# Optimization experiments

Measured on AMD Instinct MI355X. Metric: run time of the kernel, lower is better.

## Reference

```python
import jax, jax.numpy as jnp
from jax import lax
import numpy as np
import math

DIM = 192
D_INNER = DIM * 2            # 384
DT_RANK = math.ceil(DIM / 16)  # 12
D_STATE = 16
B, H, W = 4, 64, 64
KCONV = 4


def setup_inputs() -> dict:
    key = jax.random.key(0)
    ks = jax.random.split(key, 8)
    s = lambda k, shape, fan: jax.random.normal(k, shape, jnp.float32) / np.sqrt(fan).astype(np.float32)
    return {
        "x": jax.random.normal(ks[0], (B, DIM, H, W), jnp.float32),
        "W_in": s(ks[1], (2 * D_INNER, DIM), DIM),          # in_proj weight
        "conv_w": s(ks[2], (D_INNER, 1, KCONV), KCONV),     # depthwise conv weight
        "conv_b": jnp.zeros((D_INNER,), jnp.float32),
        "W_x": s(ks[3], (DT_RANK + 2 * D_STATE, D_INNER), D_INNER),  # x_proj weight
        "W_dt": s(ks[4], (D_INNER, DT_RANK), DT_RANK),      # dt_proj weight
        "b_dt": jax.random.uniform(ks[5], (D_INNER,), jnp.float32, -4.0, -2.0),  # dt_proj bias
        "A_log": jnp.tile(jnp.log(jnp.arange(1, D_STATE + 1, dtype=jnp.float32)), (D_INNER, 1)),
        "D": jnp.ones((D_INNER,), jnp.float32),
        "W_out": s(ks[6], (DIM, D_INNER), D_INNER),         # out_proj weight
    }


def _forward(x, W_in, conv_w, conv_b, W_x, W_dt, b_dt, A_log, D, W_out):
    Bb, C, Hh, Ww = x.shape
    L = Hh * Ww
    x_flat = x.reshape(Bb, C, L).transpose(0, 2, 1)        # (B, L, C)
    xz = x_flat @ W_in.T                                    # (B, L, 2*d_inner)
    x_in, z_gate = jnp.split(xz, 2, axis=-1)

    # depthwise causal conv1d: padding=3 on both sides in torch, then truncated
    # to first L outputs == left-pad-3 'VALID' conv with kernel 4.
    xt = x_in.transpose(0, 2, 1)                            # (B, d_inner, L)
    xt_pad = jnp.pad(xt, ((0, 0), (0, 0), (KCONV - 1, 0)))
    xc = lax.conv_general_dilated(
        xt_pad, conv_w, window_strides=(1,), padding="VALID",
        feature_group_count=D_INNER) + conv_b[None, :, None]
    x_conv = jax.nn.silu(xc)                                # (B, d_inner, L)

    x_dbl = jnp.einsum("bdl,kd->blk", x_conv, W_x)          # (B, L, dt_rank+32)
    dt, B_ssm, C_ssm = jnp.split(x_dbl, [DT_RANK, DT_RANK + D_STATE], axis=-1)

    # NOTE: dt_proj applies its bias AND delta_bias=dt_proj.bias is passed to the
    # scan, so the bias is added twice before softplus (faithful to source).
    dt_lin = dt @ W_dt.T + b_dt                             # (B, L, d_inner)
    delta = jax.nn.softplus(dt_lin + b_dt)

    A = -jnp.exp(A_log)                                     # (d_inner, d_state)

    # sequential selective scan over L
    def step(h, inp):
        u_t, d_t, B_t, C_t = inp                            # (B,d),(B,d),(B,n),(B,n)
        dA = jnp.exp(d_t[..., None] * A)                    # (B, d_inner, d_state)
        h = dA * h + (d_t * u_t)[..., None] * B_t[:, None, :]
        y_t = jnp.einsum("bdn,bn->bd", h, C_t)
        return h, y_t

    u_seq = x_conv.transpose(2, 0, 1)                       # (L, B, d_inner)
    d_seq = delta.transpose(1, 0, 2)                        # (L, B, d_inner)
    B_seq = B_ssm.transpose(1, 0, 2)                        # (L, B, d_state)
    C_seq = C_ssm.transpose(1, 0, 2)                        # (L, B, d_state)
    h0 = jnp.zeros((Bb, D_INNER, D_STATE), x.dtype)
    _, ys = lax.scan(step, h0, (u_seq, d_seq, B_seq, C_seq))  # (L, B, d_inner)

    y = ys.transpose(1, 2, 0) + D[None, :, None] * x_conv   # (B, d_inner, L)
    y = y * jax.nn.silu(z_gate.transpose(0, 2, 1))          # gate

    out = jnp.einsum("bdl,cd->bcl", y, W_out)               # out_proj
    return out.reshape(Bb, C, Hh, Ww)


def reference(x, W_in, conv_w, conv_b, W_x, W_dt, b_dt, A_log, D, W_out):
    return _forward(x, W_in, conv_w, conv_b, W_x, W_dt, b_dt, A_log, D, W_out)
```

## Files before the change

### kernel.cpp

```cpp
#include <hip/hip_runtime.h>
#include <hip/hip_bf16.h>
#include <math.h>

#define L_SEQ 4096
#define NB    4
#define DIMC  192
#define DIN   384
#define DIN2  768
#define DTRANK 12
#define DSTATE 16
#define NKX   44
#define G_CHUNKS 128
#define T_CHUNK  32
#define NCH  (NB*DIN*DSTATE)
#define NM   (NB*L_SEQ)
#define NBIG 448

typedef __attribute__((ext_vector_type(8))) short short8;
typedef __attribute__((ext_vector_type(4))) float floatx4;

__device__ __forceinline__ float silu_f(float v) {
    return v / (1.f + __expf(-v));
}
__device__ __forceinline__ float softplus_f(float v) {
    return fmaxf(v, 0.f) + __logf(1.f + __expf(-fabsf(v)));
}
__device__ __forceinline__ float bf2f(unsigned short u) {
    union { unsigned int i; float f; } c; c.i = ((unsigned int)u) << 16; return c.f;
}

__launch_bounds__(256)
__global__ void k_cvt_x(const float* __restrict__ x, __hip_bfloat16* __restrict__ xb) {
    __shared__ float s[32][33];
    const int b = blockIdx.z, c0 = blockIdx.y * 32, l0 = blockIdx.x * 32;
    const int tx = threadIdx.x, ty = threadIdx.y;
    const float* xp = x + ((size_t)b * DIMC + c0) * L_SEQ + l0;
#pragma unroll
    for (int r = 0; r < 4; ++r)
        s[ty + r*8][tx] = xp[(size_t)(ty + r*8) * L_SEQ + tx];
    __syncthreads();
    __hip_bfloat16* op = xb + ((size_t)b * L_SEQ + l0) * DIMC + c0;
#pragma unroll
    for (int r = 0; r < 4; ++r) {
        const int lr = ty + r*8;
        op[(size_t)lr * DIMC + tx] = __float2bfloat16(s[tx][lr]);
    }
}

#define NWI (DIN2*DIMC)
#define NWO (DIMC*DIN)
#define NWBIG (NBIG*DIN)
__launch_bounds__(256)
__global__ void k_cvt_w(const float* __restrict__ W_in, const float* __restrict__ W_out,
                        const float* __restrict__ W_x, const float* __restrict__ W_dt,
                        __hip_bfloat16* __restrict__ wbi, __hip_bfloat16* __restrict__ wbo,
                        __hip_bfloat16* __restrict__ wbig) {
    const int i = blockIdx.x * 256 + threadIdx.x;
    if (i < NWI) {
        wbi[i] = __float2bfloat16(W_in[i]);
    } else if (i < NWI + NWO) {
        const int j = i - NWI;
        wbo[j] = __float2bfloat16(W_out[j]);
    } else if (i < NWI + NWO + NWBIG) {
        const int j = i - NWI - NWO;
        const int r = j / DIN, c = j - r * DIN;
        float v;
        if (r < 32) {
            v = W_x[(size_t)(DTRANK + r) * DIN + c];
        } else if (r < 32 + DIN) {
            const int d = r - 32;
            v = 0.f;
#pragma unroll
            for (int q = 0; q < DTRANK; ++q)
                v += W_dt[d * DTRANK + q] * W_x[(size_t)q * DIN + c];
        } else {
            v = 0.f;
        }
        wbig[j] = __float2bfloat16(v);
    }
}

template<int BN, int OUTMODE>
__launch_bounds__(256)
__global__ void k_gemm(const __hip_bfloat16* __restrict__ A,
                       const __hip_bfloat16* __restrict__ B,
                       float* __restrict__ Cf, __hip_bfloat16* __restrict__ Cb,
                       float* __restrict__ Cf2, const float* __restrict__ bdt,
                       int K, int ldc) {
    constexpr int LDK = 200;
    constexpr int WN = BN / 2;
    constexpr int TN = WN / 16;
    constexpr int NCA = 6;
    constexpr int NCB = BN * 24 / 256;
    __shared__ __align__(16) __hip_bfloat16 sA[64 * LDK];
    __shared__ __align__(16) __hip_bfloat16 sB[BN * LDK];

    const int tid = threadIdx.x;
    const int lane = tid & 63;
    const int wave = tid >> 6;
    const int wm = wave >> 1, wn = wave & 1;
    const int m0 = blockIdx.x * 64;
    const int n0 = blockIdx.y * BN;
    const int mlan = lane & 15;
    const int kq8 = (lane >> 4) * 8;

    floatx4 acc[2][TN];
#pragma unroll
    for (int i = 0; i < 2; ++i)
#pragma unroll
        for (int j = 0; j < TN; ++j) acc[i][j] = (floatx4){0.f, 0.f, 0.f, 0.f};

    for (int kh = 0; kh < K; kh += 192) {
        if (kh) __syncthreads();
        uint4 va[NCA], vb[NCB];
#pragma unroll
        for (int r = 0; r < NCA; ++r) {
            const int c = r * 256 + tid, row = c / 24, cc = c - row * 24;
            va[r] = *(const uint4*)&A[(size_t)(m0 + row) * K + kh + cc * 8];
        }
#pragma unroll
        for (int r = 0; r < NCB; ++r) {
            const int c = r * 256 + tid, row = c / 24, cc = c - row * 24;
            vb[r] = *(const uint4*)&B[(size_t)(n0 + row) * K + kh + cc * 8];
        }
#pragma unroll
        for (int r = 0; r < NCA; ++r) {
            const int c = r * 256 + tid, row = c / 24, cc = c - row * 24;
            *(uint4*)&sA[row * LDK + cc * 8] = va[r];
        }
#pragma unroll
        for (int r = 0; r < NCB; ++r) {
            const int c = r * 256 + tid, row = c / 24, cc = c - row * 24;
            *(uint4*)&sB[row * LDK + cc * 8] = vb[r];
        }
        __syncthreads();
#pragma unroll
        for (int ks = 0; ks < 6; ++ks) {
            short8 af[2], bf[TN];
#pragma unroll
            for (int im = 0; im < 2; ++im)
                af[im] = *(const short8*)&sA[(wm*32 + im*16 + mlan) * LDK + ks*32 + kq8];
#pragma unroll
            for (int jn = 0; jn < TN; ++jn)
                bf[jn] = *(const short8*)&sB[(wn*WN + jn*16 + mlan) * LDK + ks*32 + kq8];
#pragma unroll
            for (int im = 0; im < 2; ++im)
#pragma unroll
                for (int jn = 0; jn < TN; ++jn)
                    acc[im][jn] = __builtin_amdgcn_mfma_f32_16x16x32_bf16(
                        af[im], bf[jn], acc[im][jn], 0, 0, 0);
        }
    }

    const int quad = lane >> 4;
#pragma unroll
    for (int im = 0; im < 2; ++im) {
#pragma unroll
        for (int jn = 0; jn < TN; ++jn) {
            const int n = n0 + wn*WN + jn*16 + mlan;
            const int mb = m0 + wm*32 + im*16 + quad*4;
#pragma unroll
            for (int r = 0; r < 4; ++r) {
                const int m = mb + r;
                const float v = acc[im][jn][r];
                if (OUTMODE == 0) {
                    Cb[(size_t)m * ldc + n] = __float2bfloat16(v);
                } else if (OUTMODE == 1) {
                    const int bb = m >> 12, ll = m & (L_SEQ - 1);
                    Cf[((size_t)bb * DIMC + n) * L_SEQ + ll] = v;
                } else {
                    if (n < 32) {
                        Cf[(size_t)m * 32 + n] = v;
                    } else if (n < 32 + DIN) {
                        Cf2[(size_t)m * DIN + (n - 32)] = softplus_f(v + 2.f * bdt[n - 32]);
                    }
                }
            }
        }
    }
}

__launch_bounds__(256)
__global__ void k_conv(const __hip_bfloat16* __restrict__ xz, const float* __restrict__ cw,
                       const float* __restrict__ cb, __hip_bfloat16* __restrict__ xcb) {
    const int idx = blockIdx.x * 256 + threadIdx.x;
    const int d = idx % DIN;
    const int m = idx / DIN;
    const int l = m & (L_SEQ - 1);
    const float4 w4 = *(const float4*)&cw[d * 4];
    float s = cb[d];
    const float w[4] = {w4.x, w4.y, w4.z, w4.w};
#pragma unroll
    for (int k = 0; k < 4; ++k) {
        const int ll = l - 3 + k;
        if (ll >= 0) s += __bfloat162float(xz[(size_t)(m - 3 + k) * DIN2 + d]) * w[k];
    }
    xcb[idx] = __float2bfloat16(silu_f(s));
}

__launch_bounds__(128)
__global__ void k_scan_a(const float* __restrict__ dlt, const __hip_bfloat16* __restrict__ xcb,
                         const float* __restrict__ xbc, const float* __restrict__ A_log,
                         float* __restrict__ S, float* __restrict__ P) {
    __shared__ float sBC[T_CHUNK * 32];
    const int tid = threadIdx.x;
    const int g = blockIdx.x, b = blockIdx.z;
    const int l0 = g * T_CHUNK;
    const size_t row0 = (size_t)b * L_SEQ + l0;
    for (int i = tid; i < T_CHUNK * 8; i += 128)
        *(float4*)&sBC[i * 4] = *(const float4*)&xbc[row0 * 32 + i * 4];
    const int d = blockIdx.y * 128 + tid;
    float dv_a[T_CHUNK];
    unsigned short uv_a[T_CHUNK];
#pragma unroll
    for (int t = 0; t < T_CHUNK; ++t)
        dv_a[t] = dlt[(row0 + t) * DIN + d];
#pragma unroll
    for (int t = 0; t < T_CHUNK; ++t)
        uv_a[t] = *(const unsigned short*)&xcb[(row0 + t) * DIN + d];
    float A[DSTATE];
#pragma unroll
    for (int n = 0; n < DSTATE; n += 4) {
        const float4 a4 = *(const float4*)&A_log[d * DSTATE + n];
        A[n] = -__expf(a4.x); A[n+1] = -__expf(a4.y);
        A[n+2] = -__expf(a4.z); A[n+3] = -__expf(a4.w);
    }
    __syncthreads();
    float h[DSTATE] = {};
    float dsum = 0.f;
#pragma unroll
    for (int t = 0; t < T_CHUNK; ++t) {
        const float dv = dv_a[t];
        const float uv = bf2f(uv_a[t]);
        const float dub = dv * uv;
        dsum += dv;
#pragma unroll
        for (int n = 0; n < DSTATE; ++n) {
            const float e = __expf(dv * A[n]);
            h[n] = e * h[n] + dub * sBC[t*32 + n];
        }
    }
    float* Sp = S + (size_t)g * NCH + (size_t)(b * DIN + d) * DSTATE;
    float* Pp = P + (size_t)g * NCH + (size_t)(b * DIN + d) * DSTATE;
#pragma unroll
    for (int n = 0; n < DSTATE; n += 4) {
        *(float4*)&Sp[n] = make_float4(h[n], h[n+1], h[n+2], h[n+3]);
        *(float4*)&Pp[n] = make_float4(__expf(A[n]*dsum), __expf(A[n+1]*dsum),
                                       __expf(A[n+2]*dsum), __expf(A[n+3]*dsum));
    }
}

__launch_bounds__(256)
__global__ void k_scan_b(float* __restrict__ Sh, const float* __restrict__ P) {
    const int ch = blockIdx.x * 256 + threadIdx.x;
    float h = 0.f;
    for (int g = 0; g < G_CHUNKS; ++g) {
        const size_t i = (size_t)g * NCH + ch;
        const float s = Sh[i];
        const float p = P[i];
        Sh[i] = h;
        h = p * h + s;
    }
}

__launch_bounds__(128)
__global__ void k_scan_c(const float* __restrict__ dlt, const __hip_bfloat16* __restrict__ xcb,
                         const float* __restrict__ xbc, const float* __restrict__ A_log,
                         const float* __restrict__ Hst, const __hip_bfloat16* __restrict__ xzb,
                         const float* __restrict__ Dv, __hip_bfloat16* __restrict__ yb) {
    __shared__ float sBC[T_CHUNK * 32];
    const int tid = threadIdx.x;
    const int g = blockIdx.x, b = blockIdx.z;
    const int l0 = g * T_CHUNK;
    const size_t row0 = (size_t)b * L_SEQ + l0;
    for (int i = tid; i < T_CHUNK * 8; i += 128)
        *(float4*)&sBC[i * 4] = *(const float4*)&xbc[row0 * 32 + i * 4];
    const int d = blockIdx.y * 128 + tid;
    float dv_a[T_CHUNK];
    unsigned short uv_a[T_CHUNK];
    unsigned short zz_a[T_CHUNK];
#pragma unroll
    for (int t = 0; t < T_CHUNK; ++t)
        dv_a[t] = dlt[(row0 + t) * DIN + d];
#pragma unroll
    for (int t = 0; t < T_CHUNK; ++t)
        uv_a[t] = *(const unsigned short*)&xcb[(row0 + t) * DIN + d];
#pragma unroll
    for (int t = 0; t < T_CHUNK; ++t)
        zz_a[t] = *(const unsigned short*)&xzb[(row0 + t) * DIN2 + DIN + d];
    float A[DSTATE];
#pragma unroll
    for (int n = 0; n < DSTATE; n += 4) {
        const float4 a4 = *(const float4*)&A_log[d * DSTATE + n];
        A[n] = -__expf(a4.x); A[n+1] = -__expf(a4.y);
        A[n+2] = -__expf(a4.z); A[n+3] = -__expf(a4.w);
    }
    float h[DSTATE];
    const float* Hp = Hst + (size_t)g * NCH + (size_t)(b * DIN + d) * DSTATE;
#pragma unroll
    for (int n = 0; n < DSTATE; n += 4) {
        const float4 h4 = *(const float4*)&Hp[n];
        h[n] = h4.x; h[n+1] = h4.y; h[n+2] = h4.z; h[n+3] = h4.w;
    }
    const float Dd = Dv[d];
    __hip_bfloat16* yl = yb + row0 * DIN + d;
    __syncthreads();
#pragma unroll
    for (int t = 0; t < T_CHUNK; ++t) {
        const float dv = dv_a[t];
        const float uv = bf2f(uv_a[t]);
        const float dub = dv * uv;
        float y0 = 0.f, y1 = 0.f, y2 = 0.f, y3 = 0.f;
#pragma unroll
        for (int n = 0; n < DSTATE; n += 4) {
            float e;
            e = __expf(dv * A[n  ]); h[n  ] = e * h[n  ] + dub * sBC[t*32 + n  ]; y0 += h[n  ] * sBC[t*32 + 16 + n  ];
            e = __expf(dv * A[n+1]); h[n+1] = e * h[n+1] + dub * sBC[t*32 + n+1]; y1 += h[n+1] * sBC[t*32 + 16 + n+1];
            e = __expf(dv * A[n+2]); h[n+2] = e * h[n+2] + dub * sBC[t*32 + n+2]; y2 += h[n+2] * sBC[t*32 + 16 + n+2];
            e = __expf(dv * A[n+3]); h[n+3] = e * h[n+3] + dub * sBC[t*32 + n+3]; y3 += h[n+3] * sBC[t*32 + 16 + n+3];
        }
        const float y = (y0 + y1) + (y2 + y3);
        yl[(size_t)t * DIN] = __float2bfloat16((y + Dd * uv) * silu_f(bf2f(zz_a[t])));
    }
}

extern "C" void kernel_launch(void* const* d_in, const int* in_sizes, int n_in,
                              void* d_out, int out_size, void* d_ws, size_t ws_size,
                              hipStream_t stream) {
    const float* x      = (const float*)d_in[0];
    const float* W_in   = (const float*)d_in[1];
    const float* conv_w = (const float*)d_in[2];
    const float* conv_b = (const float*)d_in[3];
    const float* W_x    = (const float*)d_in[4];
    const float* W_dt   = (const float*)d_in[5];
    const float* b_dt   = (const float*)d_in[6];
    const float* A_log  = (const float*)d_in[7];
    const float* Dvec   = (const float*)d_in[8];
    const float* W_out  = (const float*)d_in[9];
    float* out = (float*)d_out;

    char* p = (char*)d_ws;
    __hip_bfloat16* xb    = (__hip_bfloat16*)p; p += (size_t)NM * DIMC * 2;
    __hip_bfloat16* wbi   = (__hip_bfloat16*)p; p += (size_t)NWI * 2;
    __hip_bfloat16* wbo   = (__hip_bfloat16*)p; p += (size_t)NWO * 2;
    __hip_bfloat16* wbig  = (__hip_bfloat16*)p; p += (size_t)NWBIG * 2;
    __hip_bfloat16* xzb   = (__hip_bfloat16*)p; p += (size_t)NM * DIN2 * 2;
    __hip_bfloat16* xcb   = (__hip_bfloat16*)p; p += (size_t)NM * DIN * 2;
    float*          xbc   = (float*)p;          p += (size_t)NM * 32 * 4;
    float*          dlt   = (float*)p;          p += (size_t)NM * DIN * 4;
    __hip_bfloat16* yb    = (__hip_bfloat16*)p; p += (size_t)NM * DIN * 2;
    float*          S     = (float*)p;          p += (size_t)G_CHUNKS * NCH * 4;
    float*          P     = (float*)p;          p += (size_t)G_CHUNKS * NCH * 4;

    k_cvt_w<<<dim3((NWI + NWO + NWBIG + 255) / 256), 256, 0, stream>>>(
        W_in, W_out, W_x, W_dt, wbi, wbo, wbig);
    k_cvt_x<<<dim3(L_SEQ/32, DIMC/32, NB), dim3(32, 8), 0, stream>>>(x, xb);
    k_gemm<128, 0><<<dim3(NM/64, DIN2/128), 256, 0, stream>>>(
        xb, wbi, nullptr, xzb, nullptr, nullptr, DIMC, DIN2);
    k_conv<<<dim3((NM*(size_t)DIN)/256), 256, 0, stream>>>(xzb, conv_w, conv_b, xcb);
    k_gemm<64, 3><<<dim3(NM/64, NBIG/64), 256, 0, stream>>>(
        xcb, wbig, xbc, nullptr, dlt, b_dt, DIN, 0);
    k_scan_a<<<dim3(G_CHUNKS, 3, NB), 128, 0, stream>>>(dlt, xcb, xbc, A_log, S, P);
    k_scan_b<<<dim3(NCH/256), 256, 0, stream>>>(S, P);
    k_scan_c<<<dim3(G_CHUNKS, 3, NB), 128, 0, stream>>>(dlt, xcb, xbc, A_log,
                                                        S, xzb, Dvec, yb);
    k_gemm<96, 1><<<dim3(NM/64, DIMC/96), 256, 0, stream>>>(
        yb, wbo, out, nullptr, nullptr, nullptr, DIN, 0);
}
```

Measured before the change: 217.1 us.

## Fuse dt projection into scan kernels and fold x transpose into input GEMM

Removes the precomputed W_dt·W_x fused weight and the large fp32 delta buffer. The x_proj GEMM now writes only the 48-wide x_dbl, and both scan kernels compute delta in registers from the 12 dt-rank values with softplus. The separate x transpose/convert kernel is folded into the input GEMM, which loads fp32 x and transposes it into shared memory. This cuts a lot of global memory traffic, at the cost of recomputing the dt projection in both scan passes and doing strided scalar shared-memory stores in the input GEMM.

```diff
diff --git a/kernel.cpp b/kernel.cpp
--- a/kernel.cpp
+++ b/kernel.cpp
@@ -14,7 +14,7 @@
 #define T_CHUNK  32
 #define NCH  (NB*DIN*DSTATE)
 #define NM   (NB*L_SEQ)
-#define NBIG 448
+#define LDK  200
 
 typedef __attribute__((ext_vector_type(8))) short short8;
 typedef __attribute__((ext_vector_type(4))) float floatx4;
@@ -29,155 +29,94 @@
     union { unsigned int i; float f; } c; c.i = ((unsigned int)u) << 16; return c.f;
 }
 
-__launch_bounds__(256)
-__global__ void k_cvt_x(const float* __restrict__ x, __hip_bfloat16* __restrict__ xb) {
-    __shared__ float s[32][33];
-    const int b = blockIdx.z, c0 = blockIdx.y * 32, l0 = blockIdx.x * 32;
-    const int tx = threadIdx.x, ty = threadIdx.y;
-    const float* xp = x + ((size_t)b * DIMC + c0) * L_SEQ + l0;
-#pragma unroll
-    for (int r = 0; r < 4; ++r)
-        s[ty + r*8][tx] = xp[(size_t)(ty + r*8) * L_SEQ + tx];
-    __syncthreads();
-    __hip_bfloat16* op = xb + ((size_t)b * L_SEQ + l0) * DIMC + c0;
-#pragma unroll
-    for (int r = 0; r < 4; ++r) {
-        const int lr = ty + r*8;
-        op[(size_t)lr * DIMC + tx] = __float2bfloat16(s[tx][lr]);
-    }
-}
-
 #define NWI (DIN2*DIMC)
 #define NWO (DIMC*DIN)
-#define NWBIG (NBIG*DIN)
+#define NWX (64*DIN)
 __launch_bounds__(256)
 __global__ void k_cvt_w(const float* __restrict__ W_in, const float* __restrict__ W_out,
-                        const float* __restrict__ W_x, const float* __restrict__ W_dt,
+                        const float* __restrict__ W_x,
                         __hip_bfloat16* __restrict__ wbi, __hip_bfloat16* __restrict__ wbo,
-                        __hip_bfloat16* __restrict__ wbig) {
+                        __hip_bfloat16* __restrict__ wbx) {
     const int i = blockIdx.x * 256 + threadIdx.x;
     if (i < NWI) {
         wbi[i] = __float2bfloat16(W_in[i]);
     } else if (i < NWI + NWO) {
         const int j = i - NWI;
         wbo[j] = __float2bfloat16(W_out[j]);
-    } else if (i < NWI + NWO + NWBIG) {
+    } else if (i < NWI + NWO + NWX) {
         const int j = i - NWI - NWO;
         const int r = j / DIN, c = j - r * DIN;
-        float v;
-        if (r < 32) {
-            v = W_x[(size_t)(DTRANK + r) * DIN + c];
-        } else if (r < 32 + DIN) {
-            const int d = r - 32;
-            v = 0.f;
-#pragma unroll
-            for (int q = 0; q < DTRANK; ++q)
-                v += W_dt[d * DTRANK + q] * W_x[(size_t)q * DIN + c];
-        } else {
-            v = 0.f;
-        }
-        wbig[j] = __float2bfloat16(v);
-    }
-}
-
-template<int BN, int OUTMODE>
-__launch_bounds__(256)
-__global__ void k_gemm(const __hip_bfloat16* __restrict__ A,
-                       const __hip_bfloat16* __restrict__ B,
-                       float* __restrict__ Cf, __hip_bfloat16* __restrict__ Cb,
-                       float* __restrict__ Cf2, const float* __restrict__ bdt,
-                       int K, int ldc) {
-    constexpr int LDK = 200;
-    constexpr int WN = BN / 2;
-    constexpr int TN = WN / 16;
-    constexpr int NCA = 6;
-    constexpr int NCB = BN * 24 / 256;
+        wbx[j] = (r < NKX) ? __float2bfloat16(W_x[(size_t)r * DIN + c])
+                           : __float2bfloat16(0.f);
+    }
+}
+
+__launch_bounds__(256)
+__global__ void k_gemm_in(const float* __restrict__ x, const __hip_bfloat16* __restrict__ W,
+                          __hip_bfloat16* __restrict__ xzb) {
     __shared__ __align__(16) __hip_bfloat16 sA[64 * LDK];
-    __shared__ __align__(16) __hip_bfloat16 sB[BN * LDK];
-
+    __shared__ __align__(16) __hip_bfloat16 sB[128 * LDK];
     const int tid = threadIdx.x;
     const int lane = tid & 63;
     const int wave = tid >> 6;
     const int wm = wave >> 1, wn = wave & 1;
     const int m0 = blockIdx.x * 64;
-    const int n0 = blockIdx.y * BN;
+    const int b = m0 >> 12, l0 = m0 & (L_SEQ - 1);
+    const int n0 = blockIdx.y * 128;
     const int mlan = lane & 15;
     const int kq8 = (lane >> 4) * 8;
 
-    floatx4 acc[2][TN];
+#pragma unroll
+    for (int r = 0; r < 12; ++r) {
+        const int idx = r * 256 + tid;
+        const int c = idx >> 4, lq = (idx & 15) * 4;
+        const float4 v = *(const float4*)&x[((size_t)b * DIMC + c) * L_SEQ + l0 + lq];
+        sA[(lq + 0) * LDK + c] = __float2bfloat16(v.x);
+        sA[(lq + 1) * LDK + c] = __float2bfloat16(v.y);
+        sA[(lq + 2) * LDK + c] = __float2bfloat16(v.z);
+        sA[(lq + 3) * LDK + c] = __float2bfloat16(v.w);
+    }
+#pragma unroll
+    for (int r = 0; r < 12; ++r) {
+        const int idx = r * 256 + tid;
+        const int row = idx / 24, cc = idx % 24;
+        const uint4 wv = *(const uint4*)&W[(size_t)(n0 + row) * DIMC + cc * 8];
+        *(uint4*)&sB[row * LDK + cc * 8] = wv;
+    }
+    __syncthreads();
+
+    floatx4 acc[2][4];
 #pragma unroll
     for (int i = 0; i < 2; ++i)
 #pragma unroll
-        for (int j = 0; j < TN; ++j) acc[i][j] = (floatx4){0.f, 0.f, 0.f, 0.f};
-
-    for (int kh = 0; kh < K; kh += 192) {
-        if (kh) __syncthreads();
-        uint4 va[NCA], vb[NCB];
-#pragma unroll
-        for (int r = 0; r < NCA; ++r) {
-            const int c = r * 256 + tid, row = c / 24, cc = c - row * 24;
-            va[r] = *(const uint4*)&A[(size_t)(m0 + row) * K + kh + cc * 8];
-        }
-#pragma unroll
-        for (int r = 0; r < NCB; ++r) {
-            const int c = r * 256 + tid, row = c / 24, cc = c - row * 24;
-            vb[r] = *(const uint4*)&B[(size_t)(n0 + row) * K + kh + cc * 8];
-        }
-#pragma unroll
-        for (int r = 0; r < NCA; ++r) {
-            const int c = r * 256 + tid, row = c / 24, cc = c - row * 24;
-            *(uint4*)&sA[row * LDK + cc * 8] = va[r];
-        }
-#pragma unroll
-        for (int r = 0; r < NCB; ++r) {
-            const int c = r * 256 + tid, row = c / 24, cc = c - row * 24;
-            *(uint4*)&sB[row * LDK + cc * 8] = vb[r];
-        }
-        __syncthreads();
-#pragma unroll
-        for (int ks = 0; ks < 6; ++ks) {
-            short8 af[2], bf[TN];
-#pragma unroll
-            for (int im = 0; im < 2; ++im)
-                af[im] = *(const short8*)&sA[(wm*32 + im*16 + mlan) * LDK + ks*32 + kq8];
-#pragma unroll
-            for (int jn = 0; jn < TN; ++jn)
-                bf[jn] = *(const short8*)&sB[(wn*WN + jn*16 + mlan) * LDK + ks*32 + kq8];
-#pragma unroll
-            for (int im = 0; im < 2; ++im)
-#pragma unroll
-                for (int jn = 0; jn < TN; ++jn)
-                    acc[im][jn] = __builtin_amdgcn_mfma_f32_16x16x32_bf16(
-                        af[im], bf[jn], acc[im][jn], 0, 0, 0);
-        }
-    }
-
+        for (int j = 0; j < 4; ++j) acc[i][j] = (floatx4){0.f, 0.f, 0.f, 0.f};
+#pragma unroll
+    for (int ks = 0; ks < 6; ++ks) {
+        short8 af[2], bf[4];
+#pragma unroll
+        for (int im = 0; im < 2; ++im)
+            af[im] = *(const short8*)&sA[(wm*32 + im*16 + mlan) * LDK + ks*32 + kq8];
+#pragma unroll
+        for (int jn = 0; jn < 4; ++jn)
+            bf[jn] = *(const short8*)&sB[(wn*64 + jn*16 + mlan) * LDK + ks*32 + kq8];
+#pragma unroll
+        for (int im = 0; im < 2; ++im)
+#pragma unroll
+            for (int jn = 0; jn < 4; ++jn)
+                acc[im][jn] = __builtin_amdgcn_mfma_f32_16x16x32_bf16(
+                    af[im], bf[jn], acc[im][jn], 0, 0, 0);
+    }
     const int quad = lane >> 4;
 #pragma unroll
-    for (int im = 0; im < 2; ++im) {
-#pragma unroll
-        for (int jn = 0; jn < TN; ++jn) {
-            const int n = n0 + wn*WN + jn*16 + mlan;
+    for (int im = 0; im < 2; ++im)
+#pragma unroll
+        for (int jn = 0; jn < 4; ++jn) {
+            const int n = n0 + wn*64 + jn*16 + mlan;
             const int mb = m0 + wm*32 + im*16 + quad*4;
 #pragma unroll
-            for (int r = 0; r < 4; ++r) {
-                const int m = mb + r;
-                const float v = acc[im][jn][r];
-                if (OUTMODE == 0) {
-                    Cb[(size_t)m * ldc + n] = __float2bfloat16(v);
-                } else if (OUTMODE == 1) {
-                    const int bb = m >> 12, ll = m & (L_SEQ - 1);
-                    Cf[((size_t)bb * DIMC + n) * L_SEQ + ll] = v;
-                } else {
-                    if (n < 32) {
-                        Cf[(size_t)m * 32 + n] = v;
-                    } else if (n < 32 + DIN) {
-                        Cf2[(size_t)m * DIN + (n - 32)] = softplus_f(v + 2.f * bdt[n - 32]);
-                    }
-                }
-            }
-        }
-    }
+            for (int r = 0; r < 4; ++r)
+                xzb[(size_t)(mb + r) * DIN2 + n] = __float2bfloat16(acc[im][jn][r]);
+        }
 }
 
 __launch_bounds__(256)
@@ -198,26 +137,177 @@
     xcb[idx] = __float2bfloat16(silu_f(s));
 }
 
+__launch_bounds__(256)
+__global__ void k_gemm_xp(const __hip_bfloat16* __restrict__ A,
+                          const __hip_bfloat16* __restrict__ B,
+                          float* __restrict__ xdbl) {
+    __shared__ __align__(16) __hip_bfloat16 sA[64 * LDK];
+    __shared__ __align__(16) __hip_bfloat16 sB[64 * LDK];
+    const int tid = threadIdx.x;
+    const int lane = tid & 63;
+    const int wave = tid >> 6;
+    const int wm = wave >> 1, wn = wave & 1;
+    const int m0 = blockIdx.x * 64;
+    const int mlan = lane & 15;
+    const int kq8 = (lane >> 4) * 8;
+
+    floatx4 acc[2][2];
+#pragma unroll
+    for (int i = 0; i < 2; ++i)
+#pragma unroll
+        for (int j = 0; j < 2; ++j) acc[i][j] = (floatx4){0.f, 0.f, 0.f, 0.f};
+
+    for (int kh = 0; kh < DIN; kh += 192) {
+        uint4 va[6], vb[6];
+#pragma unroll
+        for (int r = 0; r < 6; ++r) {
+            const int idx = r * 256 + tid, row = idx / 24, cc = idx % 24;
+            va[r] = *(const uint4*)&A[(size_t)(m0 + row) * DIN + kh + cc * 8];
+            vb[r] = *(const uint4*)&B[(size_t)row * DIN + kh + cc * 8];
+        }
+        if (kh) __syncthreads();
+#pragma unroll
+        for (int r = 0; r < 6; ++r) {
+            const int idx = r * 256 + tid, row = idx / 24, cc = idx % 24;
+            *(uint4*)&sA[row * LDK + cc * 8] = va[r];
+            *(uint4*)&sB[row * LDK + cc * 8] = vb[r];
+        }
+        __syncthreads();
+#pragma unroll
+        for (int ks = 0; ks < 6; ++ks) {
+            short8 af[2], bf[2];
+#pragma unroll
+            for (int im = 0; im < 2; ++im)
+                af[im] = *(const short8*)&sA[(wm*32 + im*16 + mlan) * LDK + ks*32 + kq8];
+#pragma unroll
+            for (int jn = 0; jn < 2; ++jn)
+                bf[jn] = *(const short8*)&sB[(wn*32 + jn*16 + mlan) * LDK + ks*32 + kq8];
+#pragma unroll
+            for (int im = 0; im < 2; ++im)
+#pragma unroll
+                for (int jn = 0; jn < 2; ++jn)
+                    acc[im][jn] = __builtin_amdgcn_mfma_f32_16x16x32_bf16(
+                        af[im], bf[jn], acc[im][jn], 0, 0, 0);
+        }
+    }
+    const int quad = lane >> 4;
+#pragma unroll
+    for (int im = 0; im < 2; ++im)
+#pragma unroll
+        for (int jn = 0; jn < 2; ++jn) {
+            const int n = wn*32 + jn*16 + mlan;
+            if (n < 48) {
+                const int mb = m0 + wm*32 + im*16 + quad*4;
+#pragma unroll
+                for (int r = 0; r < 4; ++r)
+                    xdbl[(size_t)(mb + r) * 48 + n] = acc[im][jn][r];
+            }
+        }
+}
+
+__launch_bounds__(256)
+__global__ void k_gemm_out(const __hip_bfloat16* __restrict__ A,
+                           const __hip_bfloat16* __restrict__ B,
+                           float* __restrict__ out) {
+    __shared__ __align__(16) __hip_bfloat16 sA[64 * LDK];
+    __shared__ __align__(16) __hip_bfloat16 sB[96 * LDK];
+    const int tid = threadIdx.x;
+    const int lane = tid & 63;
+    const int wave = tid >> 6;
+    const int wm = wave >> 1, wn = wave & 1;
+    const int m0 = blockIdx.x * 64;
+    const int n0 = blockIdx.y * 96;
+    const int mlan = lane & 15;
+    const int kq8 = (lane >> 4) * 8;
+
+    floatx4 acc[2][3];
+#pragma unroll
+    for (int i = 0; i < 2; ++i)
+#pragma unroll
+        for (int j = 0; j < 3; ++j) acc[i][j] = (floatx4){0.f, 0.f, 0.f, 0.f};
+
+    for (int kh = 0; kh < DIN; kh += 192) {
+        uint4 va[6], vb[9];
+#pragma unroll
+        for (int r = 0; r < 6; ++r) {
+            const int idx = r * 256 + tid, row = idx / 24, cc = idx % 24;
+            va[r] = *(const uint4*)&A[(size_t)(m0 + row) * DIN + kh + cc * 8];
+        }
+#pragma unroll
+        for (int r = 0; r < 9; ++r) {
+            const int idx = r * 256 + tid, row = idx / 24, cc = idx % 24;
+            vb[r] = *(const uint4*)&B[(size_t)(n0 + row) * DIN + kh + cc * 8];
+        }
+        if (kh) __syncthreads();
+#pragma unroll
+        for (int r = 0; r < 6; ++r) {
+            const int idx = r * 256 + tid, row = idx / 24, cc = idx % 24;
+            *(uint4*)&sA[row * LDK + cc * 8] = va[r];
+        }
+#pragma unroll
+        for (int r = 0; r < 9; ++r) {
+            const int idx = r * 256 + tid, row = idx / 24, cc = idx % 24;
+            *(uint4*)&sB[row * LDK + cc * 8] = vb[r];
+        }
+        __syncthreads();
+#pragma unroll
+        for (int ks = 0; ks < 6; ++ks) {
+            short8 af[2], bf[3];
+#pragma unroll
+            for (int im = 0; im < 2; ++im)
+                af[im] = *(const short8*)&sA[(wm*32 + im*16 + mlan) * LDK + ks*32 + kq8];
+#pragma unroll
+            for (int jn = 0; jn < 3; ++jn)
+                bf[jn] = *(const short8*)&sB[(wn*48 + jn*16 + mlan) * LDK + ks*32 + kq8];
+#pragma unroll
+            for (int im = 0; im < 2; ++im)
+#pragma unroll
+                for (int jn = 0; jn < 3; ++jn)
+                    acc[im][jn] = __builtin_amdgcn_mfma_f32_16x16x32_bf16(
+                        af[im], bf[jn], acc[im][jn], 0, 0, 0);
+        }
+    }
+    const int quad = lane >> 4;
+#pragma unroll
+    for (int im = 0; im < 2; ++im)
+#pragma unroll
+        for (int jn = 0; jn < 3; ++jn) {
+            const int n = n0 + wn*48 + jn*16 + mlan;
+            const int mb = m0 + wm*32 + im*16 + quad*4;
+#pragma unroll
+            for (int r = 0; r < 4; ++r) {
+                const int m = mb + r;
+                const int bb = m >> 12, ll = m & (L_SEQ - 1);
+                out[((size_t)bb * DIMC + n) * L_SEQ + ll] = acc[im][jn][r];
+            }
+        }
+}
+
 __launch_bounds__(128)
-__global__ void k_scan_a(const float* __restrict__ dlt, const __hip_bfloat16* __restrict__ xcb,
-                         const float* __restrict__ xbc, const float* __restrict__ A_log,
+__global__ void k_scan_a(const float* __restrict__ xdbl, const __hip_bfloat16* __restrict__ xcb,
+                         const float* __restrict__ Wdt, const float* __restrict__ bdt,
+                         const float* __restrict__ A_log,
                          float* __restrict__ S, float* __restrict__ P) {
-    __shared__ float sBC[T_CHUNK * 32];
+    __shared__ float sX[T_CHUNK * 48];
     const int tid = threadIdx.x;
     const int g = blockIdx.x, b = blockIdx.z;
-    const int l0 = g * T_CHUNK;
-    const size_t row0 = (size_t)b * L_SEQ + l0;
-    for (int i = tid; i < T_CHUNK * 8; i += 128)
-        *(float4*)&sBC[i * 4] = *(const float4*)&xbc[row0 * 32 + i * 4];
+    const size_t row0 = (size_t)b * L_SEQ + g * T_CHUNK;
+    for (int i = tid; i < T_CHUNK * 12; i += 128) {
+        const int r = i / 12, q = (i % 12) * 4;
+        *(float4*)&sX[r * 48 + q] = *(const float4*)&xdbl[(row0 + r) * 48 + q];
+    }
     const int d = blockIdx.y * 128 + tid;
-    float dv_a[T_CHUNK];
     unsigned short uv_a[T_CHUNK];
-#pragma unroll
-    for (int t = 0; t < T_CHUNK; ++t)
-        dv_a[t] = dlt[(row0 + t) * DIN + d];
 #pragma unroll
     for (int t = 0; t < T_CHUNK; ++t)
         uv_a[t] = *(const unsigned short*)&xcb[(row0 + t) * DIN + d];
+    float wdt[DTRANK];
+#pragma unroll
+    for (int q = 0; q < DTRANK; q += 4) {
+        const float4 w4 = *(const float4*)&Wdt[d * DTRANK + q];
+        wdt[q] = w4.x; wdt[q+1] = w4.y; wdt[q+2] = w4.z; wdt[q+3] = w4.w;
+    }
+    const float b2 = 2.f * bdt[d];
     float A[DSTATE];
 #pragma unroll
     for (int n = 0; n < DSTATE; n += 4) {
@@ -230,14 +320,17 @@
     float dsum = 0.f;
 #pragma unroll
     for (int t = 0; t < T_CHUNK; ++t) {
-        const float dv = dv_a[t];
+        float dv = b2;
+#pragma unroll
+        for (int r = 0; r < DTRANK; ++r) dv += sX[t*48 + r] * wdt[r];
+        dv = softplus_f(dv);
         const float uv = bf2f(uv_a[t]);
         const float dub = dv * uv;
         dsum += dv;
 #pragma unroll
         for (int n = 0; n < DSTATE; ++n) {
             const float e = __expf(dv * A[n]);
-            h[n] = e * h[n] + dub * sBC[t*32 + n];
+            h[n] = e * h[n] + dub * sX[t*48 + 12 + n];
         }
     }
     float* Sp = S + (size_t)g * NCH + (size_t)(b * DIN + d) * DSTATE;
@@ -264,30 +357,35 @@
 }
 
 __launch_bounds__(128)
-__global__ void k_scan_c(const float* __restrict__ dlt, const __hip_bfloat16* __restrict__ xcb,
-                         const float* __restrict__ xbc, const float* __restrict__ A_log,
-                         const float* __restrict__ Hst, const __hip_bfloat16* __restrict__ xzb,
-                         const float* __restrict__ Dv, __hip_bfloat16* __restrict__ yb) {
-    __shared__ float sBC[T_CHUNK * 32];
+__global__ void k_scan_c(const float* __restrict__ xdbl, const __hip_bfloat16* __restrict__ xcb,
+                         const float* __restrict__ Wdt, const float* __restrict__ bdt,
+                         const float* __restrict__ A_log, const float* __restrict__ Hst,
+                         const __hip_bfloat16* __restrict__ xzb, const float* __restrict__ Dv,
+                         __hip_bfloat16* __restrict__ yb) {
+    __shared__ float sX[T_CHUNK * 48];
     const int tid = threadIdx.x;
     const int g = blockIdx.x, b = blockIdx.z;
-    const int l0 = g * T_CHUNK;
-    const size_t row0 = (size_t)b * L_SEQ + l0;
-    for (int i = tid; i < T_CHUNK * 8; i += 128)
-        *(float4*)&sBC[i * 4] = *(const float4*)&xbc[row0 * 32 + i * 4];
+    const size_t row0 = (size_t)b * L_SEQ + g * T_CHUNK;
+    for (int i = tid; i < T_CHUNK * 12; i += 128) {
+        const int r = i / 12, q = (i % 12) * 4;
+        *(float4*)&sX[r * 48 + q] = *(const float4*)&xdbl[(row0 + r) * 48 + q];
+    }
     const int d = blockIdx.y * 128 + tid;
-    float dv_a[T_CHUNK];
     unsigned short uv_a[T_CHUNK];
     unsigned short zz_a[T_CHUNK];
 #pragma unroll
     for (int t = 0; t < T_CHUNK; ++t)
-        dv_a[t] = dlt[(row0 + t) * DIN + d];
-#pragma unroll
-    for (int t = 0; t < T_CHUNK; ++t)
         uv_a[t] = *(const unsigned short*)&xcb[(row0 + t) * DIN + d];
 #pragma unroll
     for (int t = 0; t < T_CHUNK; ++t)
         zz_a[t] = *(const unsigned short*)&xzb[(row0 + t) * DIN2 + DIN + d];
+    float wdt[DTRANK];
+#pragma unroll
+    for (int q = 0; q < DTRANK; q += 4) {
+        const float4 w4 = *(const float4*)&Wdt[d * DTRANK + q];
+        wdt[q] = w4.x; wdt[q+1] = w4.y; wdt[q+2] = w4.z; wdt[q+3] = w4.w;
+    }
+    const float b2 = 2.f * bdt[d];
     float A[DSTATE];
 #pragma unroll
     for (int n = 0; n < DSTATE; n += 4) {
@@ -307,17 +405,20 @@
     __syncthreads();
 #pragma unroll
     for (int t = 0; t < T_CHUNK; ++t) {
-        const float dv = dv_a[t];
+        float dv = b2;
+#pragma unroll
+        for (int r = 0; r < DTRANK; ++r) dv += sX[t*48 + r] * wdt[r];
+        dv = softplus_f(dv);
         const float uv = bf2f(uv_a[t]);
         const float dub = dv * uv;
         float y0 = 0.f, y1 = 0.f, y2 = 0.f, y3 = 0.f;
 #pragma unroll
         for (int n = 0; n < DSTATE; n += 4) {
             float e;
-            e = __expf(dv * A[n  ]); h[n  ] = e * h[n  ] + dub * sBC[t*32 + n  ]; y0 += h[n  ] * sBC[t*32 + 16 + n  ];
-            e = __expf(dv * A[n+1]); h[n+1] = e * h[n+1] + dub * sBC[t*32 + n+1]; y1 += h[n+1] * sBC[t*32 + 16 + n+1];
-            e = __expf(dv * A[n+2]); h[n+2] = e * h[n+2] + dub * sBC[t*32 + n+2]; y2 += h[n+2] * sBC[t*32 + 16 + n+2];
-            e = __expf(dv * A[n+3]); h[n+3] = e * h[n+3] + dub * sBC[t*32 + n+3]; y3 += h[n+3] * sBC[t*32 + 16 + n+3];
+            e = __expf(dv * A[n  ]); h[n  ] = e * h[n  ] + dub * sX[t*48+12+n  ]; y0 += h[n  ] * sX[t*48+28+n  ];
+            e = __expf(dv * A[n+1]); h[n+1] = e * h[n+1] + dub * sX[t*48+12+n+1]; y1 += h[n+1] * sX[t*48+28+n+1];
+            e = __expf(dv * A[n+2]); h[n+2] = e * h[n+2] + dub * sX[t*48+12+n+2]; y2 += h[n+2] * sX[t*48+28+n+2];
+            e = __expf(dv * A[n+3]); h[n+3] = e * h[n+3] + dub * sX[t*48+12+n+3]; y3 += h[n+3] * sX[t*48+28+n+3];
         }
         const float y = (y0 + y1) + (y2 + y3);
         yl[(size_t)t * DIN] = __float2bfloat16((y + Dd * uv) * silu_f(bf2f(zz_a[t])));
@@ -340,30 +441,24 @@
     float* out = (float*)d_out;
 
     char* p = (char*)d_ws;
-    __hip_bfloat16* xb    = (__hip_bfloat16*)p; p += (size_t)NM * DIMC * 2;
-    __hip_bfloat16* wbi   = (__hip_bfloat16*)p; p += (size_t)NWI * 2;
-    __hip_bfloat16* wbo   = (__hip_bfloat16*)p; p += (size_t)NWO * 2;
-    __hip_bfloat16* wbig  = (__hip_bfloat16*)p; p += (size_t)NWBIG * 2;
-    __hip_bfloat16* xzb   = (__hip_bfloat16*)p; p += (size_t)NM * DIN2 * 2;
-    __hip_bfloat16* xcb   = (__hip_bfloat16*)p; p += (size_t)NM * DIN * 2;
-    float*          xbc   = (float*)p;          p += (size_t)NM * 32 * 4;
-    float*          dlt   = (float*)p;          p += (size_t)NM * DIN * 4;
-    __hip_bfloat16* yb    = (__hip_bfloat16*)p; p += (size_t)NM * DIN * 2;
-    float*          S     = (float*)p;          p += (size_t)G_CHUNKS * NCH * 4;
-    float*          P     = (float*)p;          p += (size_t)G_CHUNKS * NCH * 4;
-
-    k_cvt_w<<<dim3((NWI + NWO + NWBIG + 255) / 256), 256, 0, stream>>>(
-        W_in, W_out, W_x, W_dt, wbi, wbo, wbig);
-    k_cvt_x<<<dim3(L_SEQ/32, DIMC/32, NB), dim3(32, 8), 0, stream>>>(x, xb);
-    k_gemm<128, 0><<<dim3(NM/64, DIN2/128), 256, 0, stream>>>(
-        xb, wbi, nullptr, xzb, nullptr, nullptr, DIMC, DIN2);
+    __hip_bfloat16* wbi  = (__hip_bfloat16*)p; p += (size_t)NWI * 2;
+    __hip_bfloat16* wbo  = (__hip_bfloat16*)p; p += (size_t)NWO * 2;
+    __hip_bfloat16* wbx  = (__hip_bfloat16*)p; p += (size_t)NWX * 2;
+    __hip_bfloat16* xzb  = (__hip_bfloat16*)p; p += (size_t)NM * DIN2 * 2;
+    __hip_bfloat16* xcb  = (__hip_bfloat16*)p; p += (size_t)NM * DIN * 2;
+    float*          xdbl = (float*)p;          p += (size_t)NM * 48 * 4;
+    __hip_bfloat16* yb   = (__hip_bfloat16*)p; p += (size_t)NM * DIN * 2;
+    float*          S    = (float*)p;          p += (size_t)G_CHUNKS * NCH * 4;
+    float*          P    = (float*)p;          p += (size_t)G_CHUNKS * NCH * 4;
+
+    k_cvt_w<<<dim3((NWI + NWO + NWX + 255) / 256), 256, 0, stream>>>(
+        W_in, W_out, W_x, wbi, wbo, wbx);
+    k_gemm_in<<<dim3(NM/64, DIN2/128), 256, 0, stream>>>(x, wbi, xzb);
     k_conv<<<dim3((NM*(size_t)DIN)/256), 256, 0, stream>>>(xzb, conv_w, conv_b, xcb);
-    k_gemm<64, 3><<<dim3(NM/64, NBIG/64), 256, 0, stream>>>(
-        xcb, wbig, xbc, nullptr, dlt, b_dt, DIN, 0);
-    k_scan_a<<<dim3(G_CHUNKS, 3, NB), 128, 0, stream>>>(dlt, xcb, xbc, A_log, S, P);
+    k_gemm_xp<<<dim3(NM/64), 256, 0, stream>>>(xcb, wbx, xdbl);
+    k_scan_a<<<dim3(G_CHUNKS, 3, NB), 128, 0, stream>>>(xdbl, xcb, W_dt, b_dt, A_log, S, P);
     k_scan_b<<<dim3(NCH/256), 256, 0, stream>>>(S, P);
-    k_scan_c<<<dim3(G_CHUNKS, 3, NB), 128, 0, stream>>>(dlt, xcb, xbc, A_log,
+    k_scan_c<<<dim3(G_CHUNKS, 3, NB), 128, 0, stream>>>(xdbl, xcb, W_dt, b_dt, A_log,
                                                         S, xzb, Dvec, yb);
-    k_gemm<96, 1><<<dim3(NM/64, DIMC/96), 256, 0, stream>>>(
-        yb, wbo, out, nullptr, nullptr, nullptr, DIN, 0);
-}
+    k_gemm_out<<<dim3(NM/64, DIMC/96), 256, 0, stream>>>(yb, wbo, out);
+}
```

New measurement: 247.9 us. 14.2% more time.

## Store delta in bf16, drop chunk decay buffer, and stage out_proj stores via LDS

Applied to the files above, without the earlier changes.

The delta tensor is now written and read as bf16 instead of fp32, halving its traffic in the gemm epilogue and both scan kernels. The per-chunk decay tensor P is no longer stored; scan_a writes only a per-(batch,channel) delta sum, and scan_b recomputes the decay with an exp. The out_proj gemm stages its tile in shared memory so the transposed output is written as coalesced rows along L. The bf16 delta lowers precision of the step size fed into the exponential, and the extra exps in scan_b add some compute.

```diff
diff --git a/kernel.cpp b/kernel.cpp
--- a/kernel.cpp
+++ b/kernel.cpp
@@ -13,8 +13,10 @@
 #define G_CHUNKS 128
 #define T_CHUNK  32
 #define NCH  (NB*DIN*DSTATE)
+#define NBD  (NB*DIN)
 #define NM   (NB*L_SEQ)
 #define NBIG 448
+#define LDK  200
 
 typedef __attribute__((ext_vector_type(8))) short short8;
 typedef __attribute__((ext_vector_type(4))) float floatx4;
@@ -85,15 +87,16 @@
 __global__ void k_gemm(const __hip_bfloat16* __restrict__ A,
                        const __hip_bfloat16* __restrict__ B,
                        float* __restrict__ Cf, __hip_bfloat16* __restrict__ Cb,
-                       float* __restrict__ Cf2, const float* __restrict__ bdt,
+                       __hip_bfloat16* __restrict__ Cb2, const float* __restrict__ bdt,
                        int K, int ldc) {
-    constexpr int LDK = 200;
     constexpr int WN = BN / 2;
     constexpr int TN = WN / 16;
     constexpr int NCA = 6;
     constexpr int NCB = BN * 24 / 256;
-    __shared__ __align__(16) __hip_bfloat16 sA[64 * LDK];
-    __shared__ __align__(16) __hip_bfloat16 sB[BN * LDK];
+    __shared__ __align__(16) char smem[(64 + BN) * LDK * 2];
+    __hip_bfloat16* sA = (__hip_bfloat16*)smem;
+    __hip_bfloat16* sB = sA + 64 * LDK;
+    float* sOut = (float*)smem;
 
     const int tid = threadIdx.x;
     const int lane = tid & 63;
@@ -153,6 +156,29 @@
     }
 
     const int quad = lane >> 4;
+    if (OUTMODE == 1) {
+        __syncthreads();
+#pragma unroll
+        for (int im = 0; im < 2; ++im)
+#pragma unroll
+            for (int jn = 0; jn < TN; ++jn) {
+                const int nl = wn*WN + jn*16 + mlan;
+                const int ml = wm*32 + im*16 + quad*4;
+                *(float4*)&sOut[nl * 68 + ml] =
+                    make_float4(acc[im][jn][0], acc[im][jn][1],
+                                acc[im][jn][2], acc[im][jn][3]);
+            }
+        __syncthreads();
+        const int bb = m0 >> 12, l0m = m0 & (L_SEQ - 1);
+        constexpr int NIT = BN * 64 / 256;
+#pragma unroll
+        for (int it = 0; it < NIT; ++it) {
+            const int idx = it * 256 + tid;
+            const int n = idx >> 6, ml = idx & 63;
+            Cf[((size_t)bb * DIMC + n0 + n) * L_SEQ + l0m + ml] = sOut[n * 68 + ml];
+        }
+        return;
+    }
 #pragma unroll
     for (int im = 0; im < 2; ++im) {
 #pragma unroll
@@ -165,14 +191,12 @@
                 const float v = acc[im][jn][r];
                 if (OUTMODE == 0) {
                     Cb[(size_t)m * ldc + n] = __float2bfloat16(v);
-                } else if (OUTMODE == 1) {
-                    const int bb = m >> 12, ll = m & (L_SEQ - 1);
-                    Cf[((size_t)bb * DIMC + n) * L_SEQ + ll] = v;
                 } else {
                     if (n < 32) {
                         Cf[(size_t)m * 32 + n] = v;
                     } else if (n < 32 + DIN) {
-                        Cf2[(size_t)m * DIN + (n - 32)] = softplus_f(v + 2.f * bdt[n - 32]);
+                        Cb2[(size_t)m * DIN + (n - 32)] =
+                            __float2bfloat16(softplus_f(v + 2.f * bdt[n - 32]));
                     }
                 }
             }
@@ -199,22 +223,21 @@
 }
 
 __launch_bounds__(128)
-__global__ void k_scan_a(const float* __restrict__ dlt, const __hip_bfloat16* __restrict__ xcb,
+__global__ void k_scan_a(const __hip_bfloat16* __restrict__ dlt,
+                         const __hip_bfloat16* __restrict__ xcb,
                          const float* __restrict__ xbc, const float* __restrict__ A_log,
-                         float* __restrict__ S, float* __restrict__ P) {
+                         float* __restrict__ S, float* __restrict__ Dsum) {
     __shared__ float sBC[T_CHUNK * 32];
     const int tid = threadIdx.x;
     const int g = blockIdx.x, b = blockIdx.z;
-    const int l0 = g * T_CHUNK;
-    const size_t row0 = (size_t)b * L_SEQ + l0;
+    const size_t row0 = (size_t)b * L_SEQ + g * T_CHUNK;
     for (int i = tid; i < T_CHUNK * 8; i += 128)
         *(float4*)&sBC[i * 4] = *(const float4*)&xbc[row0 * 32 + i * 4];
     const int d = blockIdx.y * 128 + tid;
-    float dv_a[T_CHUNK];
-    unsigned short uv_a[T_CHUNK];
-#pragma unroll
-    for (int t = 0; t < T_CHUNK; ++t)
-        dv_a[t] = dlt[(row0 + t) * DIN + d];
+    unsigned short dv_a[T_CHUNK], uv_a[T_CHUNK];
+#pragma unroll
+    for (int t = 0; t < T_CHUNK; ++t)
+        dv_a[t] = *(const unsigned short*)&dlt[(row0 + t) * DIN + d];
 #pragma unroll
     for (int t = 0; t < T_CHUNK; ++t)
         uv_a[t] = *(const unsigned short*)&xcb[(row0 + t) * DIN + d];
@@ -230,7 +253,7 @@
     float dsum = 0.f;
 #pragma unroll
     for (int t = 0; t < T_CHUNK; ++t) {
-        const float dv = dv_a[t];
+        const float dv = bf2f(dv_a[t]);
         const float uv = bf2f(uv_a[t]);
         const float dub = dv * uv;
         dsum += dv;
@@ -241,47 +264,45 @@
         }
     }
     float* Sp = S + (size_t)g * NCH + (size_t)(b * DIN + d) * DSTATE;
-    float* Pp = P + (size_t)g * NCH + (size_t)(b * DIN + d) * DSTATE;
-#pragma unroll
-    for (int n = 0; n < DSTATE; n += 4) {
+#pragma unroll
+    for (int n = 0; n < DSTATE; n += 4)
         *(float4*)&Sp[n] = make_float4(h[n], h[n+1], h[n+2], h[n+3]);
-        *(float4*)&Pp[n] = make_float4(__expf(A[n]*dsum), __expf(A[n+1]*dsum),
-                                       __expf(A[n+2]*dsum), __expf(A[n+3]*dsum));
-    }
-}
-
-__launch_bounds__(256)
-__global__ void k_scan_b(float* __restrict__ Sh, const float* __restrict__ P) {
+    Dsum[(size_t)g * NBD + b * DIN + d] = dsum;
+}
+
+__launch_bounds__(256)
+__global__ void k_scan_b(float* __restrict__ Sh, const float* __restrict__ Dsum,
+                         const float* __restrict__ A_log) {
     const int ch = blockIdx.x * 256 + threadIdx.x;
+    const float a = -__expf(A_log[ch % (DIN * DSTATE)]);
+    const int bd = ch >> 4;
     float h = 0.f;
     for (int g = 0; g < G_CHUNKS; ++g) {
         const size_t i = (size_t)g * NCH + ch;
         const float s = Sh[i];
-        const float p = P[i];
+        const float p = __expf(a * Dsum[(size_t)g * NBD + bd]);
         Sh[i] = h;
         h = p * h + s;
     }
 }
 
 __launch_bounds__(128)
-__global__ void k_scan_c(const float* __restrict__ dlt, const __hip_bfloat16* __restrict__ xcb,
+__global__ void k_scan_c(const __hip_bfloat16* __restrict__ dlt,
+                         const __hip_bfloat16* __restrict__ xcb,
                          const float* __restrict__ xbc, const float* __restrict__ A_log,
                          const float* __restrict__ Hst, const __hip_bfloat16* __restrict__ xzb,
                          const float* __restrict__ Dv, __hip_bfloat16* __restrict__ yb) {
     __shared__ float sBC[T_CHUNK * 32];
     const int tid = threadIdx.x;
     const int g = blockIdx.x, b = blockIdx.z;
-    const int l0 = g * T_CHUNK;
-    const size_t row0 = (size_t)b * L_SEQ + l0;
+    const size_t row0 = (size_t)b * L_SEQ + g * T_CHUNK;
     for (int i = tid; i < T_CHUNK * 8; i += 128)
         *(float4*)&sBC[i * 4] = *(const float4*)&xbc[row0 * 32 + i * 4];
     const int d = blockIdx.y * 128 + tid;
-    float dv_a[T_CHUNK];
-    unsigned short uv_a[T_CHUNK];
-    unsigned short zz_a[T_CHUNK];
-#pragma unroll
-    for (int t = 0; t < T_CHUNK; ++t)
-        dv_a[t] = dlt[(row0 + t) * DIN + d];
+    unsigned short dv_a[T_CHUNK], uv_a[T_CHUNK], zz_a[T_CHUNK];
+#pragma unroll
+    for (int t = 0; t < T_CHUNK; ++t)
+        dv_a[t] = *(const unsigned short*)&dlt[(row0 + t) * DIN + d];
 #pragma unroll
     for (int t = 0; t < T_CHUNK; ++t)
         uv_a[t] = *(const unsigned short*)&xcb[(row0 + t) * DIN + d];
@@ -307,7 +328,7 @@
     __syncthreads();
 #pragma unroll
     for (int t = 0; t < T_CHUNK; ++t) {
-        const float dv = dv_a[t];
+        const float dv = bf2f(dv_a[t]);
         const float uv = bf2f(uv_a[t]);
         const float dub = dv * uv;
         float y0 = 0.f, y1 = 0.f, y2 = 0.f, y3 = 0.f;
@@ -340,17 +361,17 @@
     float* out = (float*)d_out;
 
     char* p = (char*)d_ws;
-    __hip_bfloat16* xb    = (__hip_bfloat16*)p; p += (size_t)NM * DIMC * 2;
-    __hip_bfloat16* wbi   = (__hip_bfloat16*)p; p += (size_t)NWI * 2;
-    __hip_bfloat16* wbo   = (__hip_bfloat16*)p; p += (size_t)NWO * 2;
-    __hip_bfloat16* wbig  = (__hip_bfloat16*)p; p += (size_t)NWBIG * 2;
-    __hip_bfloat16* xzb   = (__hip_bfloat16*)p; p += (size_t)NM * DIN2 * 2;
-    __hip_bfloat16* xcb   = (__hip_bfloat16*)p; p += (size_t)NM * DIN * 2;
-    float*          xbc   = (float*)p;          p += (size_t)NM * 32 * 4;
-    float*          dlt   = (float*)p;          p += (size_t)NM * DIN * 4;
-    __hip_bfloat16* yb    = (__hip_bfloat16*)p; p += (size_t)NM * DIN * 2;
-    float*          S     = (float*)p;          p += (size_t)G_CHUNKS * NCH * 4;
-    float*          P     = (float*)p;          p += (size_t)G_CHUNKS * NCH * 4;
+    __hip_bfloat16* xb   = (__hip_bfloat16*)p; p += (size_t)NM * DIMC * 2;
+    __hip_bfloat16* wbi  = (__hip_bfloat16*)p; p += (size_t)NWI * 2;
+    __hip_bfloat16* wbo  = (__hip_bfloat16*)p; p += (size_t)NWO * 2;
+    __hip_bfloat16* wbig = (__hip_bfloat16*)p; p += (size_t)NWBIG * 2;
+    __hip_bfloat16* xzb  = (__hip_bfloat16*)p; p += (size_t)NM * DIN2 * 2;
+    __hip_bfloat16* xcb  = (__hip_bfloat16*)p; p += (size_t)NM * DIN * 2;
+    float*          xbc  = (float*)p;          p += (size_t)NM * 32 * 4;
+    __hip_bfloat16* dlt  = (__hip_bfloat16*)p; p += (size_t)NM * DIN * 2;
+    __hip_bfloat16* yb   = (__hip_bfloat16*)p; p += (size_t)NM * DIN * 2;
+    float*          S    = (float*)p;          p += (size_t)G_CHUNKS * NCH * 4;
+    float*          Dsum = (float*)p;          p += (size_t)G_CHUNKS * NBD * 4;
 
     k_cvt_w<<<dim3((NWI + NWO + NWBIG + 255) / 256), 256, 0, stream>>>(
         W_in, W_out, W_x, W_dt, wbi, wbo, wbig);
@@ -360,8 +381,8 @@
     k_conv<<<dim3((NM*(size_t)DIN)/256), 256, 0, stream>>>(xzb, conv_w, conv_b, xcb);
     k_gemm<64, 3><<<dim3(NM/64, NBIG/64), 256, 0, stream>>>(
         xcb, wbig, xbc, nullptr, dlt, b_dt, DIN, 0);
-    k_scan_a<<<dim3(G_CHUNKS, 3, NB), 128, 0, stream>>>(dlt, xcb, xbc, A_log, S, P);
-    k_scan_b<<<dim3(NCH/256), 256, 0, stream>>>(S, P);
+    k_scan_a<<<dim3(G_CHUNKS, 3, NB), 128, 0, stream>>>(dlt, xcb, xbc, A_log, S, Dsum);
+    k_scan_b<<<dim3(NCH/256), 256, 0, stream>>>(S, Dsum, A_log);
     k_scan_c<<<dim3(G_CHUNKS, 3, NB), 128, 0, stream>>>(dlt, xcb, xbc, A_log,
                                                         S, xzb, Dvec, yb);
     k_gemm<96, 1><<<dim3(NM/64, DIMC/96), 256, 0, stream>>>(
```

After: 224.5 us. 1.03x slower.
